# Kernel optimization log

Hardware: AMD Instinct MI355X
Metric: run time of the kernel (lower is better)

Reference implementation:

```python
import jax, jax.numpy as jnp
import numpy as np

SPATIAL_SHAPES = [(128, 128), (64, 64), (32, 32), (16, 16)]  # sum HW = 21760
N_HEADS, N_LEVELS, N_POINTS, EMBED = 8, 4, 4, 256
HEAD_D = EMBED // N_HEADS
B, NQ = 2, 10000
NV = sum(h * w for h, w in SPATIAL_SHAPES)


def setup_inputs() -> dict:
    key = jax.random.key(0)
    ks = jax.random.split(key, 12)
    s = 0.02
    return {
        "query": jax.random.normal(ks[0], (B, NQ, EMBED), jnp.float32),
        "key": jax.random.normal(ks[1], (B, NV, EMBED), jnp.float32),
        "value": jax.random.normal(ks[2], (B, NV, EMBED), jnp.float32),
        "W_off": jax.random.normal(ks[3], (EMBED, N_HEADS * N_LEVELS * N_POINTS * 2), jnp.float32) * s,
        "b_off": jax.random.uniform(ks[4], (N_HEADS * N_LEVELS * N_POINTS * 2,), jnp.float32, -0.9, 0.9),
        "W_attn": jax.random.normal(ks[5], (EMBED, N_HEADS * N_LEVELS * N_POINTS), jnp.float32) * s,
        "b_attn": jnp.zeros((N_HEADS * N_LEVELS * N_POINTS,), jnp.float32),
        "W_v": jax.random.normal(ks[6], (EMBED, EMBED), jnp.float32) * s,
        "b_v": jnp.zeros((EMBED,), jnp.float32),
        "W_out": jax.random.normal(ks[7], (EMBED, EMBED), jnp.float32) * s,
        "b_out": jnp.zeros((EMBED,), jnp.float32),
    }


def bilinear_sample(img, gx, gy):
    """img: [N, Hs, Ws, C]; gx, gy: [N, P] in [-1, 1].
    Torch grid_sample semantics: bilinear, align_corners=True, padding_mode='zeros'.
    gx indexes width, gy indexes height."""
    N, Hs, Ws, C = img.shape
    px = (gx + 1.0) * 0.5 * (Ws - 1)
    py = (gy + 1.0) * 0.5 * (Hs - 1)
    x0 = jnp.floor(px)
    y0 = jnp.floor(py)
    wx = (px - x0)[..., None]
    wy = (py - y0)[..., None]
    x0i = x0.astype(jnp.int32)
    y0i = y0.astype(jnp.int32)
    flat = img.reshape(N, Hs * Ws, C)

    def gather(xi, yi):
        valid = ((xi >= 0) & (xi < Ws) & (yi >= 0) & (yi < Hs))[..., None]
        xc = jnp.clip(xi, 0, Ws - 1)
        yc = jnp.clip(yi, 0, Hs - 1)
        idx = yc * Ws + xc  # [N, P]
        v = jnp.take_along_axis(flat, idx[..., None], axis=1)  # [N, P, C]
        return jnp.where(valid, v, 0.0)

    v00 = gather(x0i, y0i)
    v01 = gather(x0i + 1, y0i)
    v10 = gather(x0i, y0i + 1)
    v11 = gather(x0i + 1, y0i + 1)
    top = v00 * (1.0 - wx) + v01 * wx
    bot = v10 * (1.0 - wx) + v11 * wx
    return top * (1.0 - wy) + bot * wy


def reference(query, key, value, W_off, b_off, W_attn, b_attn, W_v, b_v, W_out, b_out):
    Bq, Nq, _ = query.shape
    # value projection -> per-head values
    v = (value @ W_v + b_v).reshape(Bq, NV, N_HEADS, HEAD_D)
    # sampling locations (used directly as normalized [-1,1] grid coords) and weights
    off = (query @ W_off + b_off).reshape(Bq, Nq, N_HEADS, N_LEVELS, N_POINTS, 2)
    attn = (query @ W_attn + b_attn).reshape(Bq, Nq, N_HEADS, N_LEVELS, N_POINTS)
    attn = jax.nn.softmax(attn, axis=-1)  # softmax over points per level (as in source)

    out = jnp.zeros((Bq, Nq, EMBED), query.dtype)
    start = 0
    for lvl, (Hs, Ws) in enumerate(SPATIAL_SHAPES):
        vl = v[:, start:start + Hs * Ws].reshape(Bq, Hs, Ws, N_HEADS, HEAD_D)
        start += Hs * Ws
        vl = vl.transpose(0, 3, 1, 2, 4).reshape(Bq * N_HEADS, Hs, Ws, HEAD_D)
        gl = off[:, :, :, lvl]  # [B, Nq, H, P, 2]
        gl = gl.transpose(0, 2, 1, 3, 4).reshape(Bq * N_HEADS, Nq * N_POINTS, 2)
        samp = bilinear_sample(vl, gl[..., 0], gl[..., 1])  # [B*H, Nq*P, D]
        samp = samp.reshape(Bq, N_HEADS, Nq, N_POINTS, HEAD_D)
        wl = attn[:, :, :, lvl].transpose(0, 2, 1, 3)  # [B, H, Nq, P]
        out = out + jnp.einsum('bhqp,bhqpd->bqhd', wl, samp).reshape(Bq, Nq, EMBED)
    return out @ W_out + b_out
```

## Files before the change

### kernel.cpp

```cpp
#include <hip/hip_runtime.h>
#include <math.h>

#define B_   2
#define NQ_  10000
#define NV_  21760
#define EMB  256
#define MQ   (B_*NQ_)
#define MV   (B_*NV_)

typedef short bf16x8 __attribute__((ext_vector_type(8)));
typedef float f32x4  __attribute__((ext_vector_type(4)));

__device__ __forceinline__ unsigned short f2bf(float x) {
  unsigned u = __builtin_bit_cast(unsigned, x);
  u += 0x7FFFu + ((u >> 16) & 1u);
  return (unsigned short)(u >> 16);
}
__device__ __forceinline__ float bf2f(unsigned short s) {
  return __builtin_bit_cast(float, (unsigned)s << 16);
}

__global__ __launch_bounds__(256) void prep_weights(
    const float* __restrict__ Wv, const float* __restrict__ Wattn,
    const float* __restrict__ Woff, const float* __restrict__ Wout,
    unsigned short* __restrict__ WvT, unsigned short* __restrict__ WoutT,
    unsigned short* __restrict__ WqHi, unsigned short* __restrict__ WqLo) {
  int n = blockIdx.x;
  int k = threadIdx.x;
  if (n < 256) {
    WvT[n * 256 + k] = f2bf(Wv[k * 256 + n]);
  } else if (n < 512) {
    int c = n - 256;
    WoutT[c * 256 + k] = f2bf(Wout[k * 256 + c]);
  } else {
    int qr = n - 512;
    float x = (qr < 256) ? Woff[k * 256 + qr] : Wattn[k * 128 + (qr - 256)];
    unsigned short hi = f2bf(x);
    WqHi[qr * 256 + k] = hi;
    WqLo[qr * 256 + k] = f2bf(x - bf2f(hi));
  }
}

template <int MODE, typename OutT>
__global__ __launch_bounds__(256) void gemm_mfma(
    const void* __restrict__ Aa,
    const unsigned short* __restrict__ Bt, const unsigned short* __restrict__ Bt2,
    const float* __restrict__ bias, const float* __restrict__ bias2,
    OutT* __restrict__ C, float* __restrict__ C2, int M, int N) {
  constexpr int BM = 128, BK = 32;
  __shared__ unsigned short As[(MODE == 3 ? 2 : 1) * BM * BK];
  __shared__ unsigned short Bs[(MODE == 3 ? 2 : 1) * BM * BK];
  unsigned short* As2 = As + BM * BK;
  unsigned short* Bs2 = Bs + BM * BK;

  const int tid = threadIdx.x;
  const int lane = tid & 63, wv = tid >> 6;
  const int wr = wv >> 1, wc = wv & 1;
  const int row0 = blockIdx.x * BM, col0 = blockIdx.y * BM;

  auto lds_addr = [](int row, int kslot) -> int {
    return row * 64 + ((kslot ^ ((row >> 1) & 3)) << 4);
  };

  auto stage_bf = [&](unsigned short* dst, const unsigned short* src,
                      int rbase, int rmax, int kk) {
#pragma unroll
    for (int i = 0; i < 2; ++i) {
      int idx = tid + 256 * i;
      int row = idx >> 2, ks = idx & 3;
      int rg = min(rbase + row, rmax);
      bf16x8 vdat = *(const bf16x8*)(src + (size_t)rg * 256 + kk + ks * 8);
      *(bf16x8*)((char*)dst + lds_addr(row, ks)) = vdat;
    }
  };
  auto stage_cvt = [&](unsigned short* dst, const float* src,
                       int rbase, int rmax, int kk) {
#pragma unroll
    for (int i = 0; i < 4; ++i) {
      int idx = tid + 256 * i;
      int row = idx >> 3, c4 = idx & 7;
      int rg = min(rbase + row, rmax);
      float4 vdat = *(const float4*)(src + (size_t)rg * 256 + kk + c4 * 4);
      ushort4 o;
      o.x = f2bf(vdat.x); o.y = f2bf(vdat.y);
      o.z = f2bf(vdat.z); o.w = f2bf(vdat.w);
      *(ushort4*)((char*)dst + lds_addr(row, c4 >> 1) + (c4 & 1) * 8) = o;
    }
  };
  auto stage_cvt2 = [&](unsigned short* dstH, unsigned short* dstL,
                        const float* src, int rbase, int rmax, int kk) {
#pragma unroll
    for (int i = 0; i < 4; ++i) {
      int idx = tid + 256 * i;
      int row = idx >> 3, c4 = idx & 7;
      int rg = min(rbase + row, rmax);
      float4 vdat = *(const float4*)(src + (size_t)rg * 256 + kk + c4 * 4);
      ushort4 hh, ll;
      hh.x = f2bf(vdat.x); ll.x = f2bf(vdat.x - bf2f(hh.x));
      hh.y = f2bf(vdat.y); ll.y = f2bf(vdat.y - bf2f(hh.y));
      hh.z = f2bf(vdat.z); ll.z = f2bf(vdat.z - bf2f(hh.z));
      hh.w = f2bf(vdat.w); ll.w = f2bf(vdat.w - bf2f(hh.w));
      int a = lds_addr(row, c4 >> 1) + (c4 & 1) * 8;
      *(ushort4*)((char*)dstH + a) = hh;
      *(ushort4*)((char*)dstL + a) = ll;
    }
  };

  f32x4 acc[4][4] = {};

  for (int kk = 0; kk < 256; kk += BK) {
    if (kk) __syncthreads();
    if constexpr (MODE == 1)
      stage_cvt(As, (const float*)Aa, row0, M - 1, kk);
    else if constexpr (MODE == 3)
      stage_cvt2(As, As2, (const float*)Aa, row0, M - 1, kk);
    else
      stage_bf(As, (const unsigned short*)Aa, row0, M - 1, kk);
    stage_bf(Bs, Bt, col0, N - 1, kk);
    if constexpr (MODE == 3)
      stage_bf(Bs2, Bt2, col0, N - 1, kk);
    __syncthreads();

    const int kslot = lane >> 4;
    bf16x8 af[4], bfr[4];
#pragma unroll
    for (int i = 0; i < 4; ++i) {
      int ra = wr * 64 + i * 16 + (lane & 15);
      af[i] = *(const bf16x8*)((const char*)As + lds_addr(ra, kslot));
      int rb = wc * 64 + i * 16 + (lane & 15);
      bfr[i] = *(const bf16x8*)((const char*)Bs + lds_addr(rb, kslot));
    }
#pragma unroll
    for (int mi = 0; mi < 4; ++mi)
#pragma unroll
      for (int ni = 0; ni < 4; ++ni)
        acc[mi][ni] = __builtin_amdgcn_mfma_f32_16x16x32_bf16(
            af[mi], bfr[ni], acc[mi][ni], 0, 0, 0);

    if constexpr (MODE == 3) {
      bf16x8 af2[4], bfr2[4];
#pragma unroll
      for (int i = 0; i < 4; ++i) {
        int ra = wr * 64 + i * 16 + (lane & 15);
        af2[i] = *(const bf16x8*)((const char*)As2 + lds_addr(ra, kslot));
        int rb = wc * 64 + i * 16 + (lane & 15);
        bfr2[i] = *(const bf16x8*)((const char*)Bs2 + lds_addr(rb, kslot));
      }
#pragma unroll
      for (int mi = 0; mi < 4; ++mi)
#pragma unroll
        for (int ni = 0; ni < 4; ++ni) {
          acc[mi][ni] = __builtin_amdgcn_mfma_f32_16x16x32_bf16(
              af2[mi], bfr[ni], acc[mi][ni], 0, 0, 0);
          acc[mi][ni] = __builtin_amdgcn_mfma_f32_16x16x32_bf16(
              af[mi], bfr2[ni], acc[mi][ni], 0, 0, 0);
        }
    }
  }

#pragma unroll
  for (int ni = 0; ni < 4; ++ni) {
    int gcol = col0 + wc * 64 + ni * 16 + (lane & 15);
    float bb = (MODE == 3 && gcol >= 256) ? bias2[gcol - 256] : bias[gcol];
#pragma unroll
    for (int mi = 0; mi < 4; ++mi) {
      int rowbase = row0 + wr * 64 + mi * 16 + ((lane >> 4) << 2);
      f32x4 a = acc[mi][ni];
#pragma unroll
      for (int r = 0; r < 4; ++r) {
        int row = rowbase + r;
        if (row < M) {
          float val = a[r] + bb;
          if constexpr (MODE == 3) {
            if (gcol >= 256)
              C2[(size_t)row * 128 + (gcol - 256)] = val;
            else
              C[(size_t)row * 256 + gcol] = (OutT)val;
          } else if constexpr (sizeof(OutT) == 2) {
            C[(size_t)row * N + gcol] = (OutT)f2bf(val);
          } else {
            C[(size_t)row * N + gcol] = (OutT)val;
          }
        }
      }
    }
  }
}

__global__ __launch_bounds__(256) void msda_sample5(
    const unsigned short* __restrict__ v,
    const float* __restrict__ off,
    const float* __restrict__ attnlg,
    ushort4* __restrict__ tmp4) {
  __shared__ unsigned coeff[4 * 136 * 8];
  const int lane = threadIdx.x & 63;
  const int wq = threadIdx.x >> 6;
  const int bq = blockIdx.x * 4 + wq;
  const int b = bq / NQ_;

  unsigned* cbase = coeff + wq * (136 * 8);
  const float* offq = off + (size_t)bq * 256;
  const float* attq = attnlg + (size_t)bq * 128;

#pragma unroll
  for (int i = 0; i < 2; ++i) {
    int c = lane + i * 64;
    int h = c >> 4, l = (c >> 2) & 3, p = c & 3;
    int Wl = 128 >> l, sh = 7 - l;

    const float* lg = attq + h * 16 + l * 4;
    float l0 = lg[0], l1 = lg[1], l2 = lg[2], l3 = lg[3];
    float m = fmaxf(fmaxf(l0, l1), fmaxf(l2, l3));
    float e0 = expf(l0 - m), e1 = expf(l1 - m);
    float e2 = expf(l2 - m), e3 = expf(l3 - m);
    float ep = (p == 0) ? e0 : (p == 1) ? e1 : (p == 2) ? e2 : e3;
    float wsm = ep / (e0 + e1 + e2 + e3);

    float gx = offq[h * 32 + (l * 4 + p) * 2 + 0];
    float gy = offq[h * 32 + (l * 4 + p) * 2 + 1];
    float s = 0.5f * (float)(Wl - 1);
    float px = fmaf(gx, s, s), py = fmaf(gy, s, s);
    float x0f = floorf(px), y0f = floorf(py);
    float wx = px - x0f, wy = py - y0f;
    int x0 = (int)x0f, y0 = (int)y0f;

    bool bx0 = (unsigned)x0 < (unsigned)Wl, bx1 = (unsigned)(x0 + 1) < (unsigned)Wl;
    bool by0 = (unsigned)y0 < (unsigned)Wl, by1 = (unsigned)(y0 + 1) < (unsigned)Wl;
    int x0c = min(max(x0, 0), Wl - 1), x1c = min(max(x0 + 1, 0), Wl - 1);
    int y0c = min(max(y0, 0), Wl - 1), y1c = min(max(y0 + 1, 0), Wl - 1);

    unsigned i00 = (unsigned)((y0c << sh) + x0c), i01 = (unsigned)((y0c << sh) + x1c);
    unsigned i10 = (unsigned)((y1c << sh) + x0c), i11 = (unsigned)((y1c << sh) + x1c);

    float wxm = 1.f - wx, wym = 1.f - wy;
    float w00 = (bx0 & by0) ? wsm * wxm * wym : 0.f;
    float w01 = (bx1 & by0) ? wsm * wx  * wym : 0.f;
    float w10 = (bx0 & by1) ? wsm * wxm * wy  : 0.f;
    float w11 = (bx1 & by1) ? wsm * wx  * wy  : 0.f;

    unsigned* slot = cbase + (c + h) * 8;
    uint4 s0;
    s0.x = i00 | (i01 << 16);
    s0.y = i10 | (i11 << 16);
    s0.z = __builtin_bit_cast(unsigned, w00);
    s0.w = __builtin_bit_cast(unsigned, w01);
    *(uint4*)slot = s0;
    uint2 s1;
    s1.x = __builtin_bit_cast(unsigned, w10);
    s1.y = __builtin_bit_cast(unsigned, w11);
    *(uint2*)(slot + 4) = s1;
  }
  __syncthreads();

  const int h = lane >> 3, c4 = lane & 7;
  constexpr int LS[4] = {0, 16384, 20480, 21504};
  const char* vbase = (const char*)v;
  float4 acc = make_float4(0.f, 0.f, 0.f, 0.f);

#pragma unroll
  for (int l = 0; l < 4; ++l) {
    const unsigned lvl_off =
        ((unsigned)b * NV_ + (unsigned)LS[l]) * 512u + (unsigned)(h * 64 + c4 * 8);
    const unsigned* cb = cbase + (h * 17 + l * 4) * 8;
#pragma unroll
    for (int p = 0; p < 4; ++p) {
      uint4 s0 = *(const uint4*)(cb + p * 8);
      uint2 s1 = *(const uint2*)(cb + p * 8 + 4);
      unsigned i00 = s0.x & 0xFFFFu, i01 = s0.x >> 16;
      unsigned i10 = s0.y & 0xFFFFu, i11 = s0.y >> 16;
      float w00 = __builtin_bit_cast(float, s0.z);
      float w01 = __builtin_bit_cast(float, s0.w);
      float w10 = __builtin_bit_cast(float, s1.x);
      float w11 = __builtin_bit_cast(float, s1.y);

      uint2 r00 = *(const uint2*)(vbase + (lvl_off + (i00 << 9)));
      uint2 r01 = *(const uint2*)(vbase + (lvl_off + (i01 << 9)));
      uint2 r10 = *(const uint2*)(vbase + (lvl_off + (i10 << 9)));
      uint2 r11 = *(const uint2*)(vbase + (lvl_off + (i11 << 9)));

      acc.x += w00 * __builtin_bit_cast(float, r00.x << 16)
             + w01 * __builtin_bit_cast(float, r01.x << 16)
             + w10 * __builtin_bit_cast(float, r10.x << 16)
             + w11 * __builtin_bit_cast(float, r11.x << 16);
      acc.y += w00 * __builtin_bit_cast(float, r00.x & 0xFFFF0000u)
             + w01 * __builtin_bit_cast(float, r01.x & 0xFFFF0000u)
             + w10 * __builtin_bit_cast(float, r10.x & 0xFFFF0000u)
             + w11 * __builtin_bit_cast(float, r11.x & 0xFFFF0000u);
      acc.z += w00 * __builtin_bit_cast(float, r00.y << 16)
             + w01 * __builtin_bit_cast(float, r01.y << 16)
             + w10 * __builtin_bit_cast(float, r10.y << 16)
             + w11 * __builtin_bit_cast(float, r11.y << 16);
      acc.w += w00 * __builtin_bit_cast(float, r00.y & 0xFFFF0000u)
             + w01 * __builtin_bit_cast(float, r01.y & 0xFFFF0000u)
             + w10 * __builtin_bit_cast(float, r10.y & 0xFFFF0000u)
             + w11 * __builtin_bit_cast(float, r11.y & 0xFFFF0000u);
    }
  }
  ushort4 o;
  o.x = f2bf(acc.x); o.y = f2bf(acc.y); o.z = f2bf(acc.z); o.w = f2bf(acc.w);
  tmp4[(size_t)bq * 64 + lane] = o;
}

extern "C" void kernel_launch(void* const* d_in, const int* in_sizes, int n_in,
                              void* d_out, int out_size, void* d_ws, size_t ws_size,
                              hipStream_t stream) {
  const float* query  = (const float*)d_in[0];
  const float* value  = (const float*)d_in[2];
  const float* W_off  = (const float*)d_in[3];
  const float* b_off  = (const float*)d_in[4];
  const float* W_attn = (const float*)d_in[5];
  const float* b_attn = (const float*)d_in[6];
  const float* W_v    = (const float*)d_in[7];
  const float* b_v    = (const float*)d_in[8];
  const float* W_out  = (const float*)d_in[9];
  const float* b_out  = (const float*)d_in[10];
  float* out = (float*)d_out;

  char* p = (char*)d_ws;
  unsigned short* v_bf  = (unsigned short*)p; p += (size_t)MV * 256 * 2;
  float*          off_w = (float*)p;          p += (size_t)MQ * 256 * 4;
  float*          att_w = (float*)p;          p += (size_t)MQ * 128 * 4;
  unsigned short* tmp_bf= (unsigned short*)p; p += (size_t)MQ * 256 * 2;
  unsigned short* WvT   = (unsigned short*)p; p += 256 * 256 * 2;
  unsigned short* WoutT = (unsigned short*)p; p += 256 * 256 * 2;
  unsigned short* WqHi  = (unsigned short*)p; p += 384 * 256 * 2;
  unsigned short* WqLo  = (unsigned short*)p; p += 384 * 256 * 2;

  dim3 blk(256);

  prep_weights<<<dim3(896), blk, 0, stream>>>(
      W_v, W_attn, W_off, W_out, WvT, WoutT, WqHi, WqLo);

  gemm_mfma<1, unsigned short><<<dim3(MV / 128, 2), blk, 0, stream>>>(
      value, WvT, nullptr, b_v, nullptr, v_bf, nullptr, MV, 256);

  gemm_mfma<3, float><<<dim3((MQ + 127) / 128, 3), blk, 0, stream>>>(
      query, WqHi, WqLo, b_off, b_attn, off_w, att_w, MQ, 384);

  msda_sample5<<<dim3(MQ / 4), blk, 0, stream>>>(
      v_bf, off_w, att_w, (ushort4*)tmp_bf);

  gemm_mfma<0, float><<<dim3((MQ + 127) / 128, 2), blk, 0, stream>>>(
      tmp_bf, WoutT, nullptr, b_out, nullptr, out, nullptr, MQ, 256);
}
```

Baseline: 136.1 us.

## Store projected values in pixel-pair interleaved layout and skip split-precision for attention logits

The value-projection GEMM epilogue now writes bf16 values in a permuted layout where two horizontally adjacent pixels share a 1KB block, with each 4-channel group of the pair placed side by side. The sampler then computes byte offsets directly, so the bilinear x0/x1 corner reads fall in the same block and improve cache-line locality. Separately, the query GEMM uses the hi/lo three-term split only for the offset columns; the attention-logit columns use a single bf16 product, trading some precision for less MFMA and staging work. The permuted epilogue issues scattered 2-byte stores, which may cost write efficiency.

```diff
diff --git a/kernel.cpp b/kernel.cpp
--- a/kernel.cpp
+++ b/kernel.cpp
@@ -10,6 +10,8 @@
 
 typedef short bf16x8 __attribute__((ext_vector_type(8)));
 typedef float f32x4  __attribute__((ext_vector_type(4)));
+
+__device__ constexpr int LSc[4] = {0, 16384, 20480, 21504};
 
 __device__ __forceinline__ unsigned short f2bf(float x) {
   unsigned u = __builtin_bit_cast(unsigned, x);
@@ -41,7 +43,7 @@
   }
 }
 
-template <int MODE, typename OutT>
+template <int MODE, typename OutT, bool VPERM = false>
 __global__ __launch_bounds__(256) void gemm_mfma(
     const void* __restrict__ Aa,
     const unsigned short* __restrict__ Bt, const unsigned short* __restrict__ Bt2,
@@ -106,19 +108,24 @@
     }
   };
 
+  const bool three_term = (MODE == 3) && (col0 < 256);
+
   f32x4 acc[4][4] = {};
 
   for (int kk = 0; kk < 256; kk += BK) {
     if (kk) __syncthreads();
     if constexpr (MODE == 1)
       stage_cvt(As, (const float*)Aa, row0, M - 1, kk);
-    else if constexpr (MODE == 3)
-      stage_cvt2(As, As2, (const float*)Aa, row0, M - 1, kk);
-    else
+    else if constexpr (MODE == 3) {
+      if (three_term)
+        stage_cvt2(As, As2, (const float*)Aa, row0, M - 1, kk);
+      else
+        stage_cvt(As, (const float*)Aa, row0, M - 1, kk);
+    } else
       stage_bf(As, (const unsigned short*)Aa, row0, M - 1, kk);
     stage_bf(Bs, Bt, col0, N - 1, kk);
     if constexpr (MODE == 3)
-      stage_bf(Bs2, Bt2, col0, N - 1, kk);
+      if (three_term) stage_bf(Bs2, Bt2, col0, N - 1, kk);
     __syncthreads();
 
     const int kslot = lane >> 4;
@@ -138,48 +145,81 @@
             af[mi], bfr[ni], acc[mi][ni], 0, 0, 0);
 
     if constexpr (MODE == 3) {
-      bf16x8 af2[4], bfr2[4];
-#pragma unroll
-      for (int i = 0; i < 4; ++i) {
-        int ra = wr * 64 + i * 16 + (lane & 15);
-        af2[i] = *(const bf16x8*)((const char*)As2 + lds_addr(ra, kslot));
-        int rb = wc * 64 + i * 16 + (lane & 15);
-        bfr2[i] = *(const bf16x8*)((const char*)Bs2 + lds_addr(rb, kslot));
+      if (three_term) {
+        bf16x8 af2[4], bfr2[4];
+#pragma unroll
+        for (int i = 0; i < 4; ++i) {
+          int ra = wr * 64 + i * 16 + (lane & 15);
+          af2[i] = *(const bf16x8*)((const char*)As2 + lds_addr(ra, kslot));
+          int rb = wc * 64 + i * 16 + (lane & 15);
+          bfr2[i] = *(const bf16x8*)((const char*)Bs2 + lds_addr(rb, kslot));
+        }
+#pragma unroll
+        for (int mi = 0; mi < 4; ++mi)
+#pragma unroll
+          for (int ni = 0; ni < 4; ++ni) {
+            acc[mi][ni] = __builtin_amdgcn_mfma_f32_16x16x32_bf16(
+                af2[mi], bfr[ni], acc[mi][ni], 0, 0, 0);
+            acc[mi][ni] = __builtin_amdgcn_mfma_f32_16x16x32_bf16(
+                af[mi], bfr2[ni], acc[mi][ni], 0, 0, 0);
+          }
       }
-#pragma unroll
-      for (int mi = 0; mi < 4; ++mi)
+    }
+  }
+
+  if constexpr (VPERM) {
+    float bb4[4];
+#pragma unroll
+    for (int ni = 0; ni < 4; ++ni)
+      bb4[ni] = bias[col0 + wc * 64 + ni * 16 + (lane & 15)];
+#pragma unroll
+    for (int mi = 0; mi < 4; ++mi) {
+#pragma unroll
+      for (int r = 0; r < 4; ++r) {
+        int row = row0 + wr * 64 + mi * 16 + ((lane >> 4) << 2) + r;
+        int pix = row, bb2 = 0;
+        if (pix >= NV_) { bb2 = 1; pix -= NV_; }
+        int lvl = (pix >= 16384) + (pix >= 20480) + (pix >= 21504);
+        int sh = 7 - lvl;
+        int rel = pix - LSc[lvl];
+        int x = rel & ((1 << sh) - 1), y = rel >> sh;
+        unsigned pairoff = ((unsigned)((y << (sh - 1)) + (x >> 1)) << 10) |
+                           ((unsigned)(x & 1) << 3);
+        char* vout = (char*)C + ((size_t)bb2 * NV_ + LSc[lvl]) * 512 + pairoff;
 #pragma unroll
         for (int ni = 0; ni < 4; ++ni) {
-          acc[mi][ni] = __builtin_amdgcn_mfma_f32_16x16x32_bf16(
-              af2[mi], bfr[ni], acc[mi][ni], 0, 0, 0);
-          acc[mi][ni] = __builtin_amdgcn_mfma_f32_16x16x32_bf16(
-              af[mi], bfr2[ni], acc[mi][ni], 0, 0, 0);
+          int gcol = col0 + wc * 64 + ni * 16 + (lane & 15);
+          float val = acc[mi][ni][r] + bb4[ni];
+          int h = gcol >> 5, d = gcol & 31;
+          *(unsigned short*)(vout + h * 128 + (d >> 2) * 16 + (d & 3) * 2) =
+              f2bf(val);
         }
-    }
-  }
-
-#pragma unroll
-  for (int ni = 0; ni < 4; ++ni) {
-    int gcol = col0 + wc * 64 + ni * 16 + (lane & 15);
-    float bb = (MODE == 3 && gcol >= 256) ? bias2[gcol - 256] : bias[gcol];
-#pragma unroll
-    for (int mi = 0; mi < 4; ++mi) {
-      int rowbase = row0 + wr * 64 + mi * 16 + ((lane >> 4) << 2);
-      f32x4 a = acc[mi][ni];
-#pragma unroll
-      for (int r = 0; r < 4; ++r) {
-        int row = rowbase + r;
-        if (row < M) {
-          float val = a[r] + bb;
-          if constexpr (MODE == 3) {
-            if (gcol >= 256)
-              C2[(size_t)row * 128 + (gcol - 256)] = val;
-            else
-              C[(size_t)row * 256 + gcol] = (OutT)val;
-          } else if constexpr (sizeof(OutT) == 2) {
-            C[(size_t)row * N + gcol] = (OutT)f2bf(val);
-          } else {
-            C[(size_t)row * N + gcol] = (OutT)val;
+      }
+    }
+  } else {
+#pragma unroll
+    for (int ni = 0; ni < 4; ++ni) {
+      int gcol = col0 + wc * 64 + ni * 16 + (lane & 15);
+      float bb = (MODE == 3 && gcol >= 256) ? bias2[gcol - 256] : bias[gcol];
+#pragma unroll
+      for (int mi = 0; mi < 4; ++mi) {
+        int rowbase = row0 + wr * 64 + mi * 16 + ((lane >> 4) << 2);
+        f32x4 a = acc[mi][ni];
+#pragma unroll
+        for (int r = 0; r < 4; ++r) {
+          int row = rowbase + r;
+          if (row < M) {
+            float val = a[r] + bb;
+            if constexpr (MODE == 3) {
+              if (gcol >= 256)
+                C2[(size_t)row * 128 + (gcol - 256)] = val;
+              else
+                C[(size_t)row * 256 + gcol] = (OutT)val;
+            } else if constexpr (sizeof(OutT) == 2) {
+              C[(size_t)row * N + gcol] = (OutT)f2bf(val);
+            } else {
+              C[(size_t)row * N + gcol] = (OutT)val;
+            }
           }
         }
       }
@@ -187,8 +227,8 @@
   }
 }
 
-__global__ __launch_bounds__(256) void msda_sample5(
-    const unsigned short* __restrict__ v,
+__global__ __launch_bounds__(256) void msda_sample6(
+    const char* __restrict__ v,
     const float* __restrict__ off,
     const float* __restrict__ attnlg,
     ushort4* __restrict__ tmp4) {
@@ -196,7 +236,7 @@
   const int lane = threadIdx.x & 63;
   const int wq = threadIdx.x >> 6;
   const int bq = blockIdx.x * 4 + wq;
-  const int b = bq / NQ_;
+  const int b = (blockIdx.x * 4) / NQ_;
 
   unsigned* cbase = coeff + wq * (136 * 8);
   const float* offq = off + (size_t)bq * 256;
@@ -229,8 +269,10 @@
     int x0c = min(max(x0, 0), Wl - 1), x1c = min(max(x0 + 1, 0), Wl - 1);
     int y0c = min(max(y0, 0), Wl - 1), y1c = min(max(y0 + 1, 0), Wl - 1);
 
-    unsigned i00 = (unsigned)((y0c << sh) + x0c), i01 = (unsigned)((y0c << sh) + x1c);
-    unsigned i10 = (unsigned)((y1c << sh) + x0c), i11 = (unsigned)((y1c << sh) + x1c);
+    auto poff = [&](int xx, int yy) -> unsigned {
+      return ((unsigned)((yy << (sh - 1)) + (xx >> 1)) << 10) |
+             ((unsigned)(xx & 1) << 3);
+    };
 
     float wxm = 1.f - wx, wym = 1.f - wy;
     float w00 = (bx0 & by0) ? wsm * wxm * wym : 0.f;
@@ -240,43 +282,41 @@
 
     unsigned* slot = cbase + (c + h) * 8;
     uint4 s0;
-    s0.x = i00 | (i01 << 16);
-    s0.y = i10 | (i11 << 16);
-    s0.z = __builtin_bit_cast(unsigned, w00);
-    s0.w = __builtin_bit_cast(unsigned, w01);
+    s0.x = poff(x0c, y0c);
+    s0.y = poff(x1c, y0c);
+    s0.z = poff(x0c, y1c);
+    s0.w = poff(x1c, y1c);
     *(uint4*)slot = s0;
-    uint2 s1;
-    s1.x = __builtin_bit_cast(unsigned, w10);
-    s1.y = __builtin_bit_cast(unsigned, w11);
-    *(uint2*)(slot + 4) = s1;
+    uint4 s1;
+    s1.x = __builtin_bit_cast(unsigned, w00);
+    s1.y = __builtin_bit_cast(unsigned, w01);
+    s1.z = __builtin_bit_cast(unsigned, w10);
+    s1.w = __builtin_bit_cast(unsigned, w11);
+    *(uint4*)(slot + 4) = s1;
   }
   __syncthreads();
 
   const int h = lane >> 3, c4 = lane & 7;
-  constexpr int LS[4] = {0, 16384, 20480, 21504};
-  const char* vbase = (const char*)v;
+  const unsigned laneoff = (unsigned)(h * 128 + c4 * 16);
   float4 acc = make_float4(0.f, 0.f, 0.f, 0.f);
 
 #pragma unroll
   for (int l = 0; l < 4; ++l) {
-    const unsigned lvl_off =
-        ((unsigned)b * NV_ + (unsigned)LS[l]) * 512u + (unsigned)(h * 64 + c4 * 8);
+    const char* lb = v + ((size_t)b * NV_ + LSc[l]) * 512;
     const unsigned* cb = cbase + (h * 17 + l * 4) * 8;
 #pragma unroll
     for (int p = 0; p < 4; ++p) {
       uint4 s0 = *(const uint4*)(cb + p * 8);
-      uint2 s1 = *(const uint2*)(cb + p * 8 + 4);
-      unsigned i00 = s0.x & 0xFFFFu, i01 = s0.x >> 16;
-      unsigned i10 = s0.y & 0xFFFFu, i11 = s0.y >> 16;
-      float w00 = __builtin_bit_cast(float, s0.z);
-      float w01 = __builtin_bit_cast(float, s0.w);
-      float w10 = __builtin_bit_cast(float, s1.x);
-      float w11 = __builtin_bit_cast(float, s1.y);
-
-      uint2 r00 = *(const uint2*)(vbase + (lvl_off + (i00 << 9)));
-      uint2 r01 = *(const uint2*)(vbase + (lvl_off + (i01 << 9)));
-      uint2 r10 = *(const uint2*)(vbase + (lvl_off + (i10 << 9)));
-      uint2 r11 = *(const uint2*)(vbase + (lvl_off + (i11 << 9)));
+      uint4 s1 = *(const uint4*)(cb + p * 8 + 4);
+      float w00 = __builtin_bit_cast(float, s1.x);
+      float w01 = __builtin_bit_cast(float, s1.y);
+      float w10 = __builtin_bit_cast(float, s1.z);
+      float w11 = __builtin_bit_cast(float, s1.w);
+
+      uint2 r00 = *(const uint2*)(lb + (laneoff + s0.x));
+      uint2 r01 = *(const uint2*)(lb + (laneoff + s0.y));
+      uint2 r10 = *(const uint2*)(lb + (laneoff + s0.z));
+      uint2 r11 = *(const uint2*)(lb + (laneoff + s0.w));
 
       acc.x += w00 * __builtin_bit_cast(float, r00.x << 16)
              + w01 * __builtin_bit_cast(float, r01.x << 16)
@@ -331,14 +371,14 @@
   prep_weights<<<dim3(896), blk, 0, stream>>>(
       W_v, W_attn, W_off, W_out, WvT, WoutT, WqHi, WqLo);
 
-  gemm_mfma<1, unsigned short><<<dim3(MV / 128, 2), blk, 0, stream>>>(
+  gemm_mfma<1, unsigned short, true><<<dim3(MV / 128, 2), blk, 0, stream>>>(
       value, WvT, nullptr, b_v, nullptr, v_bf, nullptr, MV, 256);
 
   gemm_mfma<3, float><<<dim3((MQ + 127) / 128, 3), blk, 0, stream>>>(
       query, WqHi, WqLo, b_off, b_attn, off_w, att_w, MQ, 384);
 
-  msda_sample5<<<dim3(MQ / 4), blk, 0, stream>>>(
-      v_bf, off_w, att_w, (ushort4*)tmp_bf);
+  msda_sample6<<<dim3(MQ / 4), blk, 0, stream>>>(
+      (const char*)v_bf, off_w, att_w, (ushort4*)tmp_bf);
 
   gemm_mfma<0, float><<<dim3((MQ + 127) / 128, 2), blk, 0, stream>>>(
       tmp_bf, WoutT, nullptr, b_out, nullptr, out, nullptr, MQ, 256);
```

New measurement: 125.5 us. 7.8% less time.
